# Optimization experiments

Measured on AMD Instinct MI355X. Metric: run time of the kernel, lower is better.

## Reference

```python
import jax, jax.numpy as jnp
import numpy as np

B, V, H, W = 8192, 256, 128, 128  # batch, feature dim, SOM grid height/width


def setup_inputs() -> dict:
    key = jax.random.key(0)
    k1, k2 = jax.random.split(key)
    inp = jax.random.uniform(k1, (B, V), dtype=jnp.float32)
    weights = jax.random.uniform(k2, (H * W, V), dtype=jnp.float32)  # SOM codebook
    # grid node coordinates, row-major [i, j] as in the torch locations list
    ii, jj = jnp.meshgrid(jnp.arange(H), jnp.arange(W), indexing='ij')
    locations = jnp.stack([ii, jj], axis=-1).reshape(H * W, 2).astype(jnp.float32)
    return {"input": inp, "weights": weights, "locations": locations}


def reference(input, weights, locations):
    # Pairwise L2 distance between input [B,V] and codebook [N,V] via the
    x2 = jnp.sum(input * input, axis=-1, keepdims=True)        # [B,1]
    w2 = jnp.sum(weights * weights, axis=-1)                   # [N]
    d2 = x2 - 2.0 * (input @ weights.T) + w2                   # [B,N]
    dist = jnp.sqrt(jnp.maximum(d2, 0.0))
    bmu_idx = jnp.argmin(dist, axis=-1)                        # [B]
    losses = jnp.min(dist, axis=-1)                            # [B]
    bmu_locations = locations[bmu_idx]                         # [B,2]
    return bmu_locations, losses
```

## Files before the change

kernel.cpp:

```cpp
#include <hip/hip_runtime.h>
#include <stdint.h>


#define B_DIM 8192
#define V_DIM 256
#define N_DIM 16384

#define WS_W2_OFF     0
#define WS_PACKED_OFF 65536
#define WS_PLANES_OFF 131072
#define XPLANE_BYTES  (B_DIM * V_DIM * 2)
#define WPLANE_BYTES  (N_DIM * V_DIM * 2)
#define WS_FAST_NEED  (WS_PLANES_OFF + 2 * XPLANE_BYTES + 2 * WPLANE_BYTES)

typedef __attribute__((ext_vector_type(8))) short short8;
typedef __attribute__((ext_vector_type(4))) float f32x4;

__device__ __forceinline__ unsigned long long packKey(float s, unsigned idx) {
    unsigned u = __float_as_uint(s);
    u = (u & 0x80000000u) ? ~u : (u | 0x80000000u);
    return ((unsigned long long)u << 32) | (unsigned long long)idx;
}

__global__ __launch_bounds__(256) void w2_kernel(const float* __restrict__ W,
                                                 float* __restrict__ w2) {
    int lane = threadIdx.x & 63;
    int wv   = threadIdx.x >> 6;
    int n    = blockIdx.x * 4 + wv;
    float4 v = ((const float4*)(W + (size_t)n * V_DIM))[lane];
    float s = v.x * v.x + v.y * v.y + v.z * v.z + v.w * v.w;
    #pragma unroll
    for (int m = 32; m >= 1; m >>= 1) s += __shfl_xor(s, m);
    if (lane == 0) w2[n] = s;
}


__device__ __forceinline__ unsigned bfrn(float x) {
    unsigned u = __float_as_uint(x);
    return (u + 0x7FFFu + ((u >> 16) & 1u)) >> 16;
}
__device__ __forceinline__ float bf2f(unsigned h) { return __uint_as_float(h << 16); }

__global__ __launch_bounds__(256) void convert_planes(const float* __restrict__ X,
                                                      const float* __restrict__ W,
                                                      unsigned short* __restrict__ Xh,
                                                      unsigned short* __restrict__ Xl,
                                                      unsigned short* __restrict__ Wh,
                                                      unsigned short* __restrict__ Wl) {
    int gid = blockIdx.x * 256 + threadIdx.x;
    int s   = gid & 31;
    int row = gid >> 5;
    const float* src;
    unsigned short *dh, *dl;
    int r;
    if (row < B_DIM) { r = row; src = X + (size_t)r * V_DIM; dh = Xh; dl = Xl; }
    else             { r = row - B_DIM; src = W + (size_t)r * V_DIM; dh = Wh; dl = Wl; }

    float4 a = ((const float4*)src)[s * 2];
    float4 b = ((const float4*)src)[s * 2 + 1];
    float v[8] = {a.x, a.y, a.z, a.w, b.x, b.y, b.z, b.w};
    unsigned hi[8], lo[8];
    #pragma unroll
    for (int i = 0; i < 8; ++i) {
        hi[i] = bfrn(v[i]);
        lo[i] = bfrn(v[i] - bf2f(hi[i]));
    }
    uint4 hp, lp;
    hp.x = hi[0] | (hi[1] << 16); hp.y = hi[2] | (hi[3] << 16);
    hp.z = hi[4] | (hi[5] << 16); hp.w = hi[6] | (hi[7] << 16);
    lp.x = lo[0] | (lo[1] << 16); lp.y = lo[2] | (lo[3] << 16);
    lp.z = lo[4] | (lo[5] << 16); lp.w = lo[6] | (lo[7] << 16);

    int sp = (s & ~3) | ((s & 3) ^ ((r >> 1) & 3));
    *(uint4*)(dh + (size_t)r * V_DIM + sp * 8) = hp;
    *(uint4*)(dl + (size_t)r * V_DIM + sp * 8) = lp;
}

__device__ __forceinline__ void gl16(const void* g, void* l) {
    __builtin_amdgcn_global_load_lds((const __attribute__((address_space(1))) unsigned int*)g,
                                     (__attribute__((address_space(3))) unsigned int*)l,
                                     16, 0, 0);
}

#define BM 128
#define BN 128
#define FBK 32
#define FKSTEPS (V_DIM / FBK)

__global__ __launch_bounds__(256) void som_fast(const unsigned short* __restrict__ Xh,
                                                const unsigned short* __restrict__ Xl,
                                                const unsigned short* __restrict__ Wh,
                                                const unsigned short* __restrict__ Wl,
                                                const float* __restrict__ w2,
                                                unsigned long long* __restrict__ packed) {
    __shared__ char lds[32768];
    char* Ah = lds;
    char* Al = lds + 8192;
    char* Bh = lds + 16384;
    char* Bl = lds + 24576;

    const int t    = threadIdx.x;
    const int lane = t & 63;
    const int wv   = t >> 6;
    const int wr   = wv >> 1, wc = wv & 1;
    const int fr   = lane & 15;
    const int kq   = lane >> 4;

    const int rb = blockIdx.x >> 7;
    const int cb = blockIdx.x & 127;
    const int r0 = rb * BM, c0 = cb * BN;

    const size_t aOff = (size_t)(r0 + (t >> 2)) * V_DIM + (t & 3) * 8;
    const size_t bOff = (size_t)(c0 + (t >> 2)) * V_DIM + (t & 3) * 8;
    const unsigned short* sXh = Xh + aOff;
    const unsigned short* sXl = Xl + aOff;
    const unsigned short* sWh = Wh + bOff;
    const unsigned short* sWl = Wl + bOff;
    const int t16 = t * 16;

#define ISSUE(ks)                                                          \
    do {                                                                   \
        gl16(sXh + (ks) * FBK,            Ah + t16);                       \
        gl16(sXh + 64 * V_DIM + (ks) * FBK, Ah + 4096 + t16);              \
        gl16(sXl + (ks) * FBK,            Al + t16);                       \
        gl16(sXl + 64 * V_DIM + (ks) * FBK, Al + 4096 + t16);              \
        gl16(sWh + (ks) * FBK,            Bh + t16);                       \
        gl16(sWh + 64 * V_DIM + (ks) * FBK, Bh + 4096 + t16);              \
        gl16(sWl + (ks) * FBK,            Bl + t16);                       \
        gl16(sWl + 64 * V_DIM + (ks) * FBK, Bl + 4096 + t16);              \
    } while (0)

    f32x4 acc[4][4];
    #pragma unroll
    for (int i = 0; i < 4; ++i)
        #pragma unroll
        for (int j = 0; j < 4; ++j)
            acc[i][j] = (f32x4){0.f, 0.f, 0.f, 0.f};

    ISSUE(0);

    for (int ks = 0; ks < FKSTEPS; ++ks) {
        __syncthreads();

        short8 fah[4], fal[4], fbh[4], fbl[4];
        #pragma unroll
        for (int i = 0; i < 4; ++i) {
            const int row = wr * 64 + i * 16 + fr;
            const int off = row * 64 + ((kq ^ ((row >> 1) & 3)) << 4);
            fah[i] = *(const short8*)(Ah + off);
            fal[i] = *(const short8*)(Al + off);
        }
        #pragma unroll
        for (int j = 0; j < 4; ++j) {
            const int col = wc * 64 + j * 16 + fr;
            const int off = col * 64 + ((kq ^ ((col >> 1) & 3)) << 4);
            fbh[j] = *(const short8*)(Bh + off);
            fbl[j] = *(const short8*)(Bl + off);
        }
        __syncthreads();

        if (ks + 1 < FKSTEPS) ISSUE(ks + 1);

        #pragma unroll
        for (int i = 0; i < 4; ++i)
            #pragma unroll
            for (int j = 0; j < 4; ++j) {
                acc[i][j] = __builtin_amdgcn_mfma_f32_16x16x32_bf16(fah[i], fbh[j], acc[i][j], 0, 0, 0);
                acc[i][j] = __builtin_amdgcn_mfma_f32_16x16x32_bf16(fah[i], fbl[j], acc[i][j], 0, 0, 0);
                acc[i][j] = __builtin_amdgcn_mfma_f32_16x16x32_bf16(fal[i], fbh[j], acc[i][j], 0, 0, 0);
            }
    }
#undef ISSUE

    float w2v[4];
    #pragma unroll
    for (int j = 0; j < 4; ++j) w2v[j] = w2[c0 + wc * 64 + j * 16 + fr];

    #pragma unroll
    for (int i = 0; i < 4; ++i) {
        #pragma unroll
        for (int r = 0; r < 4; ++r) {
            const int row = r0 + wr * 64 + i * 16 + kq * 4 + r;
            float best = 3.4e38f;
            unsigned bidx = 0u;
            #pragma unroll
            for (int j = 0; j < 4; ++j) {
                const unsigned n = (unsigned)(c0 + wc * 64 + j * 16 + fr);
                const float s = fmaf(-2.0f, acc[i][j][r], w2v[j]);
                if (s < best) { best = s; bidx = n; }
            }
            #pragma unroll
            for (int m = 1; m <= 8; m <<= 1) {
                float    ov = __shfl_xor(best, m);
                unsigned oi = (unsigned)__shfl_xor((int)bidx, m);
                if (ov < best || (ov == best && oi < bidx)) { best = ov; bidx = oi; }
            }
            if (fr == 0) atomicMin(&packed[row], packKey(best, bidx));
        }
    }
}


__device__ __forceinline__ unsigned packhi2(float a, float b) {
    return (__float_as_uint(a) >> 16) | (__float_as_uint(b) & 0xFFFF0000u);
}
__device__ __forceinline__ unsigned packlo2(float a, float b) {
    float ah = __uint_as_float(__float_as_uint(a) & 0xFFFF0000u);
    float bh = __uint_as_float(__float_as_uint(b) & 0xFFFF0000u);
    return (__float_as_uint(a - ah) >> 16) | (__float_as_uint(b - bh) & 0xFFFF0000u);
}
__device__ __forceinline__ uint4 mku4(unsigned a, unsigned b, unsigned c, unsigned d) {
    uint4 r; r.x = a; r.y = b; r.z = c; r.w = d; return r;
}
__device__ __forceinline__ uint4 hi8(float4 p, float4 q) {
    return mku4(packhi2(p.x, p.y), packhi2(p.z, p.w), packhi2(q.x, q.y), packhi2(q.z, q.w));
}
__device__ __forceinline__ uint4 lo8(float4 p, float4 q) {
    return mku4(packlo2(p.x, p.y), packlo2(p.z, p.w), packlo2(q.x, q.y), packlo2(q.z, q.w));
}
__device__ __forceinline__ int lb(int row, int slot) {
    return row * 64 + ((slot ^ ((row >> 1) & 3)) << 4);
}

__global__ __launch_bounds__(256, 2) void som_mfma(const float* __restrict__ X,
                                                   const float* __restrict__ W,
                                                   const float* __restrict__ w2,
                                                   unsigned long long* __restrict__ packed) {
    __shared__ char lds[4 * 8192];
    char* Ahp = lds;
    char* Alp = lds + 8192;
    char* Bhp = lds + 16384;
    char* Blp = lds + 24576;

    const int t     = threadIdx.x;
    const int lane  = t & 63;
    const int wv    = t >> 6;
    const int wr    = wv >> 1, wc = wv & 1;
    const int fr    = lane & 15;
    const int kslot = lane >> 4;

    const int rb = blockIdx.x >> 7;
    const int cb = blockIdx.x & 127;
    const int r0 = rb * BM, c0 = cb * BN;

    const int sr = t >> 1;
    const int sh = t & 1;
    const float* xg = (const float*)X + (size_t)(r0 + sr) * V_DIM + sh * 16;
    const float* wg = (const float*)W + (size_t)(c0 + sr) * V_DIM + sh * 16;

    float4 pa[4], pb[4];
    #pragma unroll
    for (int q = 0; q < 4; ++q) { pa[q] = ((const float4*)xg)[q]; pb[q] = ((const float4*)wg)[q]; }

    f32x4 acc[4][4];
    #pragma unroll
    for (int i = 0; i < 4; ++i)
        #pragma unroll
        for (int j = 0; j < 4; ++j) acc[i][j] = (f32x4){0.f, 0.f, 0.f, 0.f};

    for (int ks = 0; ks < 8; ++ks) {
        uint4 cah0 = hi8(pa[0], pa[1]), cah1 = hi8(pa[2], pa[3]);
        uint4 cal0 = lo8(pa[0], pa[1]), cal1 = lo8(pa[2], pa[3]);
        uint4 cbh0 = hi8(pb[0], pb[1]), cbh1 = hi8(pb[2], pb[3]);
        uint4 cbl0 = lo8(pb[0], pb[1]), cbl1 = lo8(pb[2], pb[3]);

        __syncthreads();
        *(uint4*)(Ahp + lb(sr, 2 * sh))     = cah0;
        *(uint4*)(Ahp + lb(sr, 2 * sh + 1)) = cah1;
        *(uint4*)(Alp + lb(sr, 2 * sh))     = cal0;
        *(uint4*)(Alp + lb(sr, 2 * sh + 1)) = cal1;
        *(uint4*)(Bhp + lb(sr, 2 * sh))     = cbh0;
        *(uint4*)(Bhp + lb(sr, 2 * sh + 1)) = cbh1;
        *(uint4*)(Blp + lb(sr, 2 * sh))     = cbl0;
        *(uint4*)(Blp + lb(sr, 2 * sh + 1)) = cbl1;
        __syncthreads();

        if (ks + 1 < 8) {
            const float* xn = xg + (ks + 1) * 32;
            const float* wn = wg + (ks + 1) * 32;
            #pragma unroll
            for (int q = 0; q < 4; ++q) { pa[q] = ((const float4*)xn)[q]; pb[q] = ((const float4*)wn)[q]; }
        }

        short8 fah[4], fal[4], fbh[4], fbl[4];
        #pragma unroll
        for (int i = 0; i < 4; ++i) {
            int row = wr * 64 + i * 16 + fr;
            fah[i] = *(const short8*)(Ahp + lb(row, kslot));
            fal[i] = *(const short8*)(Alp + lb(row, kslot));
        }
        #pragma unroll
        for (int j = 0; j < 4; ++j) {
            int col = wc * 64 + j * 16 + fr;
            fbh[j] = *(const short8*)(Bhp + lb(col, kslot));
            fbl[j] = *(const short8*)(Blp + lb(col, kslot));
        }
        #pragma unroll
        for (int i = 0; i < 4; ++i)
            #pragma unroll
            for (int j = 0; j < 4; ++j) {
                acc[i][j] = __builtin_amdgcn_mfma_f32_16x16x32_bf16(fah[i], fbh[j], acc[i][j], 0, 0, 0);
                acc[i][j] = __builtin_amdgcn_mfma_f32_16x16x32_bf16(fah[i], fbl[j], acc[i][j], 0, 0, 0);
                acc[i][j] = __builtin_amdgcn_mfma_f32_16x16x32_bf16(fal[i], fbh[j], acc[i][j], 0, 0, 0);
            }
    }

    float w2v[4];
    #pragma unroll
    for (int j = 0; j < 4; ++j) w2v[j] = w2[c0 + wc * 64 + j * 16 + fr];

    #pragma unroll
    for (int i = 0; i < 4; ++i) {
        #pragma unroll
        for (int r = 0; r < 4; ++r) {
            const int row = r0 + wr * 64 + i * 16 + kslot * 4 + r;
            float best = 3.4e38f;
            unsigned bidx = 0u;
            #pragma unroll
            for (int j = 0; j < 4; ++j) {
                const unsigned n = (unsigned)(c0 + wc * 64 + j * 16 + fr);
                const float s = fmaf(-2.0f, acc[i][j][r], w2v[j]);
                if (s < best) { best = s; bidx = n; }
            }
            #pragma unroll
            for (int m = 1; m <= 8; m <<= 1) {
                float    ov = __shfl_xor(best, m);
                unsigned oi = (unsigned)__shfl_xor((int)bidx, m);
                if (ov < best || (ov == best && oi < bidx)) { best = ov; bidx = oi; }
            }
            if (fr == 0) atomicMin(&packed[row], packKey(best, bidx));
        }
    }
}

__global__ __launch_bounds__(256) void finalize(const float* __restrict__ X,
                                                const float* __restrict__ loc,
                                                const unsigned long long* __restrict__ packed,
                                                float* __restrict__ out) {
    int lane = threadIdx.x & 63;
    int wv   = threadIdx.x >> 6;
    int b    = blockIdx.x * 4 + wv;
    float4 v = ((const float4*)(X + (size_t)b * V_DIM))[lane];
    float x2 = v.x * v.x + v.y * v.y + v.z * v.z + v.w * v.w;
    #pragma unroll
    for (int m = 32; m >= 1; m >>= 1) x2 += __shfl_xor(x2, m);
    if (lane == 0) {
        unsigned long long p = packed[b];
        unsigned key = (unsigned)(p >> 32);
        unsigned idx = (unsigned)(p & 0xFFFFFFFFu);
        unsigned sb  = (key & 0x80000000u) ? (key & 0x7FFFFFFFu) : ~key;
        float s  = __uint_as_float(sb);
        float d2 = fmaxf(x2 + s, 0.0f);
        out[2 * b]     = loc[2 * idx];
        out[2 * b + 1] = loc[2 * idx + 1];
        out[2 * B_DIM + b] = sqrtf(d2);
    }
}

extern "C" void kernel_launch(void* const* d_in, const int* in_sizes, int n_in,
                              void* d_out, int out_size, void* d_ws, size_t ws_size,
                              hipStream_t stream) {
    const float* X = (const float*)d_in[0];
    const float* W = (const float*)d_in[1];
    const float* L = (const float*)d_in[2];
    float* out = (float*)d_out;

    float* w2 = (float*)((char*)d_ws + WS_W2_OFF);
    unsigned long long* packed = (unsigned long long*)((char*)d_ws + WS_PACKED_OFF);

    hipMemsetAsync(packed, 0xFF, B_DIM * sizeof(unsigned long long), stream);
    w2_kernel<<<N_DIM / 4, 256, 0, stream>>>(W, w2);

    if (ws_size >= (size_t)WS_FAST_NEED) {
        unsigned short* Xh = (unsigned short*)((char*)d_ws + WS_PLANES_OFF);
        unsigned short* Xl = (unsigned short*)((char*)Xh + XPLANE_BYTES);
        unsigned short* Wh = (unsigned short*)((char*)Xl + XPLANE_BYTES);
        unsigned short* Wl = (unsigned short*)((char*)Wh + WPLANE_BYTES);
        convert_planes<<<(B_DIM + N_DIM) * 32 / 256, 256, 0, stream>>>(X, W, Xh, Xl, Wh, Wl);
        som_fast<<<(B_DIM / BM) * (N_DIM / BN), 256, 0, stream>>>(Xh, Xl, Wh, Wl, w2, packed);
    } else {
        som_mfma<<<(B_DIM / BM) * (N_DIM / BN), 256, 0, stream>>>(X, W, w2, packed);
    }
    finalize<<<B_DIM / 4, 256, 0, stream>>>(X, L, packed, out);
}
```

Measured before the change: 286.8 us.

## Enlarge GEMM tile to 256x256 with double-buffered LDS and block swizzle

The split-bf16 MFMA distance kernel now uses 256x256 output tiles with 512 threads (8 waves, 2x4), a 128KB double-buffered LDS pipeline with explicit vmcnt waits, and a block-index swizzle for L2 locality. The larger tiles give each loaded byte more reuse, and the prefetch of the next K-slice now overlaps with compute. In exchange it uses more LDS and registers per block (acc doubles to 8x4), which lowers occupancy. The hand-written waitcnt and barrier sequence is also fragile.

```diff
diff --git a/kernel.cpp b/kernel.cpp
--- a/kernel.cpp
+++ b/kernel.cpp
@@ -82,74 +82,82 @@
                                      16, 0, 0);
 }
 
-#define BM 128
-#define BN 128
+#define FBM 256
+#define FBN 256
 #define FBK 32
 #define FKSTEPS (V_DIM / FBK)
 
-__global__ __launch_bounds__(256) void som_fast(const unsigned short* __restrict__ Xh,
-                                                const unsigned short* __restrict__ Xl,
-                                                const unsigned short* __restrict__ Wh,
-                                                const unsigned short* __restrict__ Wl,
-                                                const float* __restrict__ w2,
-                                                unsigned long long* __restrict__ packed) {
-    __shared__ char lds[32768];
-    char* Ah = lds;
-    char* Al = lds + 8192;
-    char* Bh = lds + 16384;
-    char* Bl = lds + 24576;
+__global__ __launch_bounds__(512, 2) void som_fast(const unsigned short* __restrict__ Xh,
+                                                   const unsigned short* __restrict__ Xl,
+                                                   const unsigned short* __restrict__ Wh,
+                                                   const unsigned short* __restrict__ Wl,
+                                                   const float* __restrict__ w2,
+                                                   unsigned long long* __restrict__ packed) {
+    __shared__ __align__(16) char lds[131072];
 
     const int t    = threadIdx.x;
     const int lane = t & 63;
     const int wv   = t >> 6;
-    const int wr   = wv >> 1, wc = wv & 1;
+    const int wr   = wv >> 2;
+    const int wc   = wv & 3;
     const int fr   = lane & 15;
     const int kq   = lane >> 4;
 
-    const int rb = blockIdx.x >> 7;
-    const int cb = blockIdx.x & 127;
-    const int r0 = rb * BM, c0 = cb * BN;
-
-    const size_t aOff = (size_t)(r0 + (t >> 2)) * V_DIM + (t & 3) * 8;
-    const size_t bOff = (size_t)(c0 + (t >> 2)) * V_DIM + (t & 3) * 8;
-    const unsigned short* sXh = Xh + aOff;
-    const unsigned short* sXl = Xl + aOff;
-    const unsigned short* sWh = Wh + bOff;
-    const unsigned short* sWl = Wl + bOff;
+    const int bid = blockIdx.x;
+    const int swz = (bid & 7) * 256 + (bid >> 3);
+    const int rb = swz >> 6;
+    const int cb = swz & 63;
+    const int r0 = rb * FBM, c0 = cb * FBN;
+
+    const char* pXh = (const char*)Xh + (((size_t)(r0 + (t >> 2))) << 9) + ((t & 3) << 4);
+    const char* pXl = (const char*)Xl + (((size_t)(r0 + (t >> 2))) << 9) + ((t & 3) << 4);
+    const char* pWh = (const char*)Wh + (((size_t)(c0 + (t >> 2))) << 9) + ((t & 3) << 4);
+    const char* pWl = (const char*)Wl + (((size_t)(c0 + (t >> 2))) << 9) + ((t & 3) << 4);
     const int t16 = t * 16;
 
-#define ISSUE(ks)                                                          \
-    do {                                                                   \
-        gl16(sXh + (ks) * FBK,            Ah + t16);                       \
-        gl16(sXh + 64 * V_DIM + (ks) * FBK, Ah + 4096 + t16);              \
-        gl16(sXl + (ks) * FBK,            Al + t16);                       \
-        gl16(sXl + 64 * V_DIM + (ks) * FBK, Al + 4096 + t16);              \
-        gl16(sWh + (ks) * FBK,            Bh + t16);                       \
-        gl16(sWh + 64 * V_DIM + (ks) * FBK, Bh + 4096 + t16);              \
-        gl16(sWl + (ks) * FBK,            Bl + t16);                       \
-        gl16(sWl + 64 * V_DIM + (ks) * FBK, Bl + 4096 + t16);              \
+#define ISSUE(ks, B)                                              \
+    do {                                                          \
+        gl16(pXh + (ks) * 64,         (B) + t16);                 \
+        gl16(pXh + 65536 + (ks) * 64, (B) + 8192 + t16);          \
+        gl16(pXl + (ks) * 64,         (B) + 16384 + t16);         \
+        gl16(pXl + 65536 + (ks) * 64, (B) + 24576 + t16);         \
+        gl16(pWh + (ks) * 64,         (B) + 32768 + t16);         \
+        gl16(pWh + 65536 + (ks) * 64, (B) + 40960 + t16);         \
+        gl16(pWl + (ks) * 64,         (B) + 49152 + t16);         \
+        gl16(pWl + 65536 + (ks) * 64, (B) + 57344 + t16);         \
     } while (0)
 
-    f32x4 acc[4][4];
-    #pragma unroll
-    for (int i = 0; i < 4; ++i)
+    f32x4 acc[8][4];
+    #pragma unroll
+    for (int i = 0; i < 8; ++i)
         #pragma unroll
         for (int j = 0; j < 4; ++j)
             acc[i][j] = (f32x4){0.f, 0.f, 0.f, 0.f};
 
-    ISSUE(0);
+    char* buf0 = lds;
+    char* buf1 = lds + 65536;
+
+    ISSUE(0, buf0);
 
     for (int ks = 0; ks < FKSTEPS; ++ks) {
-        __syncthreads();
-
-        short8 fah[4], fal[4], fbh[4], fbl[4];
-        #pragma unroll
-        for (int i = 0; i < 4; ++i) {
-            const int row = wr * 64 + i * 16 + fr;
-            const int off = row * 64 + ((kq ^ ((row >> 1) & 3)) << 4);
-            fah[i] = *(const short8*)(Ah + off);
-            fal[i] = *(const short8*)(Al + off);
-        }
+        char* cur = (ks & 1) ? buf1 : buf0;
+        char* nxt = (ks & 1) ? buf0 : buf1;
+
+        if (ks + 1 < FKSTEPS) {
+            ISSUE(ks + 1, nxt);
+            asm volatile("s_waitcnt vmcnt(8)" ::: "memory");
+        } else {
+            asm volatile("s_waitcnt vmcnt(0)" ::: "memory");
+        }
+        __builtin_amdgcn_s_barrier();
+        __builtin_amdgcn_sched_barrier(0);
+
+        const char* Ah = cur;
+        const char* Al = cur + 16384;
+        const char* Bh = cur + 32768;
+        const char* Bl = cur + 49152;
+
+        short8 fbh[4], fbl[4];
         #pragma unroll
         for (int j = 0; j < 4; ++j) {
             const int col = wc * 64 + j * 16 + fr;
@@ -157,18 +165,21 @@
             fbh[j] = *(const short8*)(Bh + off);
             fbl[j] = *(const short8*)(Bl + off);
         }
-        __syncthreads();
-
-        if (ks + 1 < FKSTEPS) ISSUE(ks + 1);
-
-        #pragma unroll
-        for (int i = 0; i < 4; ++i)
+        #pragma unroll
+        for (int i = 0; i < 8; ++i) {
+            const int row = wr * 128 + i * 16 + fr;
+            const int off = row * 64 + ((kq ^ ((row >> 1) & 3)) << 4);
+            short8 fah = *(const short8*)(Ah + off);
+            short8 fal = *(const short8*)(Al + off);
             #pragma unroll
             for (int j = 0; j < 4; ++j) {
-                acc[i][j] = __builtin_amdgcn_mfma_f32_16x16x32_bf16(fah[i], fbh[j], acc[i][j], 0, 0, 0);
-                acc[i][j] = __builtin_amdgcn_mfma_f32_16x16x32_bf16(fah[i], fbl[j], acc[i][j], 0, 0, 0);
-                acc[i][j] = __builtin_amdgcn_mfma_f32_16x16x32_bf16(fal[i], fbh[j], acc[i][j], 0, 0, 0);
-            }
+                acc[i][j] = __builtin_amdgcn_mfma_f32_16x16x32_bf16(fah, fbh[j], acc[i][j], 0, 0, 0);
+                acc[i][j] = __builtin_amdgcn_mfma_f32_16x16x32_bf16(fah, fbl[j], acc[i][j], 0, 0, 0);
+                acc[i][j] = __builtin_amdgcn_mfma_f32_16x16x32_bf16(fal, fbh[j], acc[i][j], 0, 0, 0);
+            }
+        }
+        asm volatile("s_waitcnt lgkmcnt(0)" ::: "memory");
+        __builtin_amdgcn_s_barrier();
     }
 #undef ISSUE
 
@@ -177,10 +188,10 @@
     for (int j = 0; j < 4; ++j) w2v[j] = w2[c0 + wc * 64 + j * 16 + fr];
 
     #pragma unroll
-    for (int i = 0; i < 4; ++i) {
+    for (int i = 0; i < 8; ++i) {
         #pragma unroll
         for (int r = 0; r < 4; ++r) {
-            const int row = r0 + wr * 64 + i * 16 + kq * 4 + r;
+            const int row = r0 + wr * 128 + i * 16 + kq * 4 + r;
             float best = 3.4e38f;
             unsigned bidx = 0u;
             #pragma unroll
@@ -241,7 +252,7 @@
 
     const int rb = blockIdx.x >> 7;
     const int cb = blockIdx.x & 127;
-    const int r0 = rb * BM, c0 = cb * BN;
+    const int r0 = rb * 128, c0 = cb * 128;
 
     const int sr = t >> 1;
     const int sh = t & 1;
@@ -377,9 +388,9 @@
         unsigned short* Wh = (unsigned short*)((char*)Xl + XPLANE_BYTES);
         unsigned short* Wl = (unsigned short*)((char*)Wh + WPLANE_BYTES);
         convert_planes<<<(B_DIM + N_DIM) * 32 / 256, 256, 0, stream>>>(X, W, Xh, Xl, Wh, Wl);
-        som_fast<<<(B_DIM / BM) * (N_DIM / BN), 256, 0, stream>>>(Xh, Xl, Wh, Wl, w2, packed);
+        som_fast<<<(B_DIM / FBM) * (N_DIM / FBN), 512, 0, stream>>>(Xh, Xl, Wh, Wl, w2, packed);
     } else {
-        som_mfma<<<(B_DIM / BM) * (N_DIM / BN), 256, 0, stream>>>(X, W, w2, packed);
+        som_mfma<<<(B_DIM / 128) * (N_DIM / 128), 256, 0, stream>>>(X, W, w2, packed);
     }
     finalize<<<B_DIM / 4, 256, 0, stream>>>(X, L, packed, out);
 }
```

Result: slower. 388.7 us (+35.5%).

## Double-buffer LDS tiles in som_fast with XCD-aware block swizzle

Applied to the files above, without the earlier changes.

Replaces the single-buffered LDS tile load in som_fast with a two-stage double buffer. The next K-step's global→LDS loads are issued before the current step's fragments are read, and explicit vmcnt waits and barriers replace __syncthreads. Block indices are remapped so each XCD works on a compact group of row/column tiles for better L2 reuse, and MFMA sections raise wave priority. LDS use doubles to 64KB per block with launch_bounds(256,2), which may limit occupancy. The hand-written waitcnt and barrier sequencing must stay correct.

```diff
diff --git a/kernel.cpp b/kernel.cpp
--- a/kernel.cpp
+++ b/kernel.cpp
@@ -82,22 +82,17 @@
                                      16, 0, 0);
 }
 
-#define BM 128
-#define BN 128
-#define FBK 32
-#define FKSTEPS (V_DIM / FBK)
-
-__global__ __launch_bounds__(256) void som_fast(const unsigned short* __restrict__ Xh,
-                                                const unsigned short* __restrict__ Xl,
-                                                const unsigned short* __restrict__ Wh,
-                                                const unsigned short* __restrict__ Wl,
-                                                const float* __restrict__ w2,
-                                                unsigned long long* __restrict__ packed) {
-    __shared__ char lds[32768];
-    char* Ah = lds;
-    char* Al = lds + 8192;
-    char* Bh = lds + 16384;
-    char* Bl = lds + 24576;
+#define BARX()   asm volatile("s_barrier" ::: "memory")
+#define VMC8()   asm volatile("s_waitcnt vmcnt(8)" ::: "memory")
+#define VMC0()   asm volatile("s_waitcnt vmcnt(0)" ::: "memory")
+
+__global__ __launch_bounds__(256, 2) void som_fast(const unsigned short* __restrict__ Xh,
+                                                   const unsigned short* __restrict__ Xl,
+                                                   const unsigned short* __restrict__ Wh,
+                                                   const unsigned short* __restrict__ Wl,
+                                                   const float* __restrict__ w2,
+                                                   unsigned long long* __restrict__ packed) {
+    __shared__ __align__(16) char lds[65536];
 
     const int t    = threadIdx.x;
     const int lane = t & 63;
@@ -106,28 +101,30 @@
     const int fr   = lane & 15;
     const int kq   = lane >> 4;
 
-    const int rb = blockIdx.x >> 7;
-    const int cb = blockIdx.x & 127;
-    const int r0 = rb * BM, c0 = cb * BN;
-
-    const size_t aOff = (size_t)(r0 + (t >> 2)) * V_DIM + (t & 3) * 8;
-    const size_t bOff = (size_t)(c0 + (t >> 2)) * V_DIM + (t & 3) * 8;
-    const unsigned short* sXh = Xh + aOff;
-    const unsigned short* sXl = Xl + aOff;
-    const unsigned short* sWh = Wh + bOff;
-    const unsigned short* sWl = Wl + bOff;
+    const int bid = blockIdx.x;
+    const int xcd = bid & 7;
+    const int q   = bid >> 3;
+    const int w   = q >> 5;
+    const int rb  = xcd * 8 + (w & 1) * 4 + ((q >> 3) & 3);
+    const int cb  = (w >> 1) * 8 + (q & 7);
+    const int r0 = rb * 128, c0 = cb * 128;
+
+    const char* pXh = (const char*)Xh + (((size_t)(r0 + (t >> 2))) << 9) + ((t & 3) << 4);
+    const char* pXl = (const char*)Xl + (((size_t)(r0 + (t >> 2))) << 9) + ((t & 3) << 4);
+    const char* pWh = (const char*)Wh + (((size_t)(c0 + (t >> 2))) << 9) + ((t & 3) << 4);
+    const char* pWl = (const char*)Wl + (((size_t)(c0 + (t >> 2))) << 9) + ((t & 3) << 4);
     const int t16 = t * 16;
 
-#define ISSUE(ks)                                                          \
-    do {                                                                   \
-        gl16(sXh + (ks) * FBK,            Ah + t16);                       \
-        gl16(sXh + 64 * V_DIM + (ks) * FBK, Ah + 4096 + t16);              \
-        gl16(sXl + (ks) * FBK,            Al + t16);                       \
-        gl16(sXl + 64 * V_DIM + (ks) * FBK, Al + 4096 + t16);              \
-        gl16(sWh + (ks) * FBK,            Bh + t16);                       \
-        gl16(sWh + 64 * V_DIM + (ks) * FBK, Bh + 4096 + t16);              \
-        gl16(sWl + (ks) * FBK,            Bl + t16);                       \
-        gl16(sWl + 64 * V_DIM + (ks) * FBK, Bl + 4096 + t16);              \
+#define ISSUE(kk, B)                                            \
+    do {                                                        \
+        gl16(pXh + (kk) * 64,         (B) + t16);               \
+        gl16(pXh + 32768 + (kk) * 64, (B) + 4096  + t16);       \
+        gl16(pXl + (kk) * 64,         (B) + 8192  + t16);       \
+        gl16(pXl + 32768 + (kk) * 64, (B) + 12288 + t16);       \
+        gl16(pWh + (kk) * 64,         (B) + 16384 + t16);       \
+        gl16(pWh + 32768 + (kk) * 64, (B) + 20480 + t16);       \
+        gl16(pWl + (kk) * 64,         (B) + 24576 + t16);       \
+        gl16(pWl + 32768 + (kk) * 64, (B) + 28672 + t16);       \
     } while (0)
 
     f32x4 acc[4][4];
@@ -137,30 +134,37 @@
         for (int j = 0; j < 4; ++j)
             acc[i][j] = (f32x4){0.f, 0.f, 0.f, 0.f};
 
-    ISSUE(0);
-
-    for (int ks = 0; ks < FKSTEPS; ++ks) {
-        __syncthreads();
+    char* buf0 = lds;
+    char* buf1 = lds + 32768;
+
+    ISSUE(0, buf0);
+
+    #pragma unroll
+    for (int ks = 0; ks < 8; ++ks) {
+        char* cur = (ks & 1) ? buf1 : buf0;
+        char* nxt = (ks & 1) ? buf0 : buf1;
+
+        BARX();
+        if (ks < 7) { ISSUE(ks + 1, nxt); VMC8(); }
+        else        { VMC0(); }
+        BARX();
 
         short8 fah[4], fal[4], fbh[4], fbl[4];
+        #pragma unroll
+        for (int j = 0; j < 4; ++j) {
+            const int col = wc * 64 + j * 16 + fr;
+            const int off = col * 64 + ((kq ^ ((col >> 1) & 3)) << 4);
+            fbh[j] = *(const short8*)(cur + 16384 + off);
+            fbl[j] = *(const short8*)(cur + 24576 + off);
+        }
         #pragma unroll
         for (int i = 0; i < 4; ++i) {
             const int row = wr * 64 + i * 16 + fr;
             const int off = row * 64 + ((kq ^ ((row >> 1) & 3)) << 4);
-            fah[i] = *(const short8*)(Ah + off);
-            fal[i] = *(const short8*)(Al + off);
-        }
-        #pragma unroll
-        for (int j = 0; j < 4; ++j) {
-            const int col = wc * 64 + j * 16 + fr;
-            const int off = col * 64 + ((kq ^ ((col >> 1) & 3)) << 4);
-            fbh[j] = *(const short8*)(Bh + off);
-            fbl[j] = *(const short8*)(Bl + off);
-        }
-        __syncthreads();
-
-        if (ks + 1 < FKSTEPS) ISSUE(ks + 1);
-
+            fah[i] = *(const short8*)(cur + off);
+            fal[i] = *(const short8*)(cur + 8192 + off);
+        }
+        __builtin_amdgcn_s_setprio(1);
         #pragma unroll
         for (int i = 0; i < 4; ++i)
             #pragma unroll
@@ -169,6 +173,7 @@
                 acc[i][j] = __builtin_amdgcn_mfma_f32_16x16x32_bf16(fah[i], fbl[j], acc[i][j], 0, 0, 0);
                 acc[i][j] = __builtin_amdgcn_mfma_f32_16x16x32_bf16(fal[i], fbh[j], acc[i][j], 0, 0, 0);
             }
+        __builtin_amdgcn_s_setprio(0);
     }
 #undef ISSUE
 
@@ -241,7 +246,7 @@
 
     const int rb = blockIdx.x >> 7;
     const int cb = blockIdx.x & 127;
-    const int r0 = rb * BM, c0 = cb * BN;
+    const int r0 = rb * 128, c0 = cb * 128;
 
     const int sr = t >> 1;
     const int sh = t & 1;
@@ -377,9 +382,9 @@
         unsigned short* Wh = (unsigned short*)((char*)Xl + XPLANE_BYTES);
         unsigned short* Wl = (unsigned short*)((char*)Wh + WPLANE_BYTES);
         convert_planes<<<(B_DIM + N_DIM) * 32 / 256, 256, 0, stream>>>(X, W, Xh, Xl, Wh, Wl);
-        som_fast<<<(B_DIM / BM) * (N_DIM / BN), 256, 0, stream>>>(Xh, Xl, Wh, Wl, w2, packed);
+        som_fast<<<(B_DIM / 128) * (N_DIM / 128), 256, 0, stream>>>(Xh, Xl, Wh, Wl, w2, packed);
     } else {
-        som_mfma<<<(B_DIM / BM) * (N_DIM / BN), 256, 0, stream>>>(X, W, w2, packed);
+        som_mfma<<<(B_DIM / 128) * (N_DIM / 128), 256, 0, stream>>>(X, W, w2, packed);
     }
     finalize<<<B_DIM / 4, 256, 0, stream>>>(X, L, packed, out);
 }
```

Result: faster. 272.4 us (-5.0%).
